# Kernel tuning notes

Measured on AMD Instinct MI355X. Metric: run time of the kernel, lower is better.

Reference implementation:

```python
import jax, jax.numpy as jnp
import numpy as np

EPS = 1e-5  # torch BatchNorm default eps


def _bn(x, gamma, beta, axes):
    # training-mode batch norm over `axes`, channel dim is axis 1
    mean = jnp.mean(x, axis=axes, keepdims=True)
    var = jnp.var(x, axis=axes, keepdims=True)
    shape = [1] * x.ndim
    shape[1] = -1
    return (x - mean) * jax.lax.rsqrt(var + EPS) * gamma.reshape(shape) + beta.reshape(shape)


def setup_inputs() -> dict:
    B, C, N = 16, 512, 192
    S_RATIO, R_RATIO = 4, 8
    Cs, Cr = C // S_RATIO, C // R_RATIO  # 128, 64
    inter = N * Cr + C  # 12800
    key = jax.random.key(0)
    ks = jax.random.split(key, 6)

    def w(k, shp, fan):
        return jax.random.normal(k, shp, jnp.float32) * np.float32(np.sqrt(2.0 / fan))

    return {
        "inputs": jax.random.normal(ks[0], (B, C, N), jnp.float32),
        "retain": 0,
        "theta_w": w(ks[1], (Cs, C), Cs), "theta_b": jnp.zeros((Cs,), jnp.float32),
        "theta_g": jnp.ones((Cs,), jnp.float32), "theta_be": jnp.zeros((Cs,), jnp.float32),
        "phi_w": w(ks[2], (Cs, C), Cs), "phi_b": jnp.zeros((Cs,), jnp.float32),
        "phi_g": jnp.ones((Cs,), jnp.float32), "phi_be": jnp.zeros((Cs,), jnp.float32),
        "re_w": w(ks[3], (Cr, Cs), Cr), "re_b": jnp.zeros((Cr,), jnp.float32),
        "re_g": jnp.ones((Cr,), jnp.float32), "re_be": jnp.zeros((Cr,), jnp.float32),
        "att_w": w(ks[4], (C, inter), C), "att_b": jnp.zeros((C,), jnp.float32),
        "att_g": jnp.ones((C,), jnp.float32), "att_be": jnp.zeros((C,), jnp.float32),
    }


def reference(inputs, retain, theta_w, theta_b, theta_g, theta_be,
              phi_w, phi_b, phi_g, phi_be, re_w, re_b, re_g, re_be,
              att_w, att_b, att_g, att_be):
    B, C, N = inputs.shape
    xt = inputs.transpose(0, 2, 1)  # [B, N, C]

    # theta / phi pro_blocks: Linear -> BN1d (over B,N) -> ReLU, output [B, Cs, N]
    th = jax.nn.relu(_bn(jnp.einsum('bnc,oc->bon', xt, theta_w) + theta_b[None, :, None], theta_g, theta_be, (0, 2)))
    ph = jax.nn.relu(_bn(jnp.einsum('bnc,oc->bon', xt, phi_w) + phi_b[None, :, None], phi_g, phi_be, (0, 2)))
    th = th.transpose(0, 2, 1)  # [B, N, Cs]
    ph = ph.transpose(0, 2, 1)  # [B, N, Cs]

    # pairwise broadcast-diff: [B, N, N, Cs]
    diff = th[:, :, None, :] - ph[:, None, :, :]

    # pro_block1: Linear -> BN2d -> ReLU, then flatten to [B, N, N*Cr]
    rel = jnp.einsum('bijc,oc->boij', diff, re_w) + re_b[None, :, None, None]  # [B, Cr, N, N]
    rel = jax.nn.relu(_bn(rel, re_g, re_be, (0, 2, 3)))
    rel = rel.transpose(0, 2, 3, 1).reshape(B, N, -1)  # [B, N, N*Cr]

    # attention_generator: Linear -> BN1d -> sigmoid, output [B, C, N]
    cat = jnp.concatenate([xt, rel], axis=2)  # [B, N, C + N*Cr]
    att = jnp.einsum('bni,oi->bon', cat, att_w) + att_b[None, :, None]  # [B, C, N]
    att = jax.nn.sigmoid(_bn(att, att_g, att_be, (0, 2)))

    features = att * inputs  # [B, C, N]
    if retain:
        return features
    return jnp.sum(features, axis=2) / jnp.sum(att, axis=2)  # [B, C]
```

## Files before the change

kernel.cpp:

```cpp
#include <hip/hip_runtime.h>

#define BB 16
#define CC 512
#define NN 192
#define CS 128
#define CR 64
#define EPSF 1e-5f
#define PART (BB*CC*NN)

typedef __attribute__((ext_vector_type(8))) short short8;
typedef __attribute__((ext_vector_type(4))) float f32x4;
typedef __attribute__((ext_vector_type(4))) unsigned int uint4v;

#define OFF_LIN2  0
#define OFF_P2    786432
#define OFF_QT    983040
#define OFF_ATTP4 1179648
#define OFF_WBF   7471104
#define OFF_XT    10747904
#define OFF_ROWS  11534336
#define OFF_SPART 11567104

__device__ __forceinline__ unsigned pkbf(float a, float b){
  unsigned r; asm("v_cvt_pk_bf16_f32 %0, %1, %2" : "=v"(r) : "v"(a), "v"(b)); return r;
}

__device__ __forceinline__ void gload_lds16(const void* g, void* l){
  __builtin_amdgcn_global_load_lds(
      (const __attribute__((address_space(1))) unsigned int*)g,
      (__attribute__((address_space(3))) unsigned int*)l, 16, 0, 0);
}

__global__ __launch_bounds__(256) void kconvxt(
    const float* __restrict__ aw, const float* __restrict__ x,
    short* __restrict__ wbf, short* __restrict__ xT)
{
  __shared__ float Ts[64][65];
  int tid = threadIdx.x;
  if (blockIdx.x < 3200) {
    int base = blockIdx.x * 2048;
    int i0 = base + tid*4;
    int i1 = base + 1024 + tid*4;
    float4 v0 = *reinterpret_cast<const float4*>(&aw[i0]);
    float4 v1 = *reinterpret_cast<const float4*>(&aw[i1]);
    uint2 w0 = make_uint2(pkbf(v0.x,v0.y), pkbf(v0.z,v0.w));
    uint2 w1 = make_uint2(pkbf(v1.x,v1.y), pkbf(v1.z,v1.w));
    *reinterpret_cast<uint2*>(&wbf[i0]) = w0;
    *reinterpret_cast<uint2*>(&wbf[i1]) = w1;
  } else {
    int bid = blockIdx.x - 3200;
    int nt = bid % 3; int ct = (bid/3) & 7; int b = bid / 24;
    int c0 = ct*64, n0 = nt*64;
    int col = tid & 63, r0 = tid >> 6;
    #pragma unroll
    for (int it = 0; it < 16; ++it){
      int r = r0 + it*4;
      Ts[r][col] = x[(b*CC + c0 + r)*NN + n0 + col];
    }
    __syncthreads();
    #pragma unroll
    for (int it = 0; it < 2; ++it){
      int cp = it*256 + tid;
      int nr = cp >> 3, cc8 = (cp & 7)*8;
      uint4v wv;
      wv.x = pkbf(Ts[cc8+0][nr], Ts[cc8+1][nr]);
      wv.y = pkbf(Ts[cc8+2][nr], Ts[cc8+3][nr]);
      wv.z = pkbf(Ts[cc8+4][nr], Ts[cc8+5][nr]);
      wv.w = pkbf(Ts[cc8+6][nr], Ts[cc8+7][nr]);
      *reinterpret_cast<uint4v*>(&xT[((b*NN) + n0 + nr)*CC + c0 + cc8]) = wv;
    }
  }
}

__global__ __launch_bounds__(256) void k1_lin(
    const float* __restrict__ x, const float* __restrict__ wth,
    const float* __restrict__ wph, float* __restrict__ lin2,
    float* __restrict__ spart)
{
  int bid = blockIdx.x;
  int nt = bid % 3; int ch = (bid/3) & 3; int b = (bid/12) & 15; int path = bid/192;
  int cs0 = ch*32, n0 = nt*64;
  const float* w = path ? wph : wth;
  int tid = threadIdx.x;
  int ty = tid >> 4, tx = tid & 15;
  __shared__ float Xs[32][64];
  __shared__ float Ws[32][36];
  float acc[2][4];
  #pragma unroll
  for (int i=0;i<2;++i)
    #pragma unroll
    for (int j=0;j<4;++j) acc[i][j]=0.f;
  for (int c0 = 0; c0 < CC; c0 += 32){
    __syncthreads();
    {
      int nn4 = (tid & 15)*4, cb = tid >> 4;
      *reinterpret_cast<float4*>(&Xs[cb][nn4]) =
        *reinterpret_cast<const float4*>(&x[(b*CC + c0 + cb)*NN + n0 + nn4]);
      *reinterpret_cast<float4*>(&Xs[cb+16][nn4]) =
        *reinterpret_cast<const float4*>(&x[(b*CC + c0 + cb + 16)*NN + n0 + nn4]);
    }
    {
      int cc = tid & 31, sb = tid >> 5;
      #pragma unroll
      for (int it = 0; it < 4; ++it)
        Ws[cc][sb + it*8] = w[(cs0 + sb + it*8)*CC + c0 + cc];
    }
    __syncthreads();
    #pragma unroll 8
    for (int cc = 0; cc < 32; ++cc){
      float w2[2], x4[4];
      w2[0] = Ws[cc][ty*2]; w2[1] = Ws[cc][ty*2+1];
      *reinterpret_cast<float4*>(x4) = *reinterpret_cast<const float4*>(&Xs[cc][tx*4]);
      #pragma unroll
      for (int i=0;i<2;++i)
        #pragma unroll
        for (int j=0;j<4;++j) acc[i][j] += w2[i]*x4[j];
    }
  }
  #pragma unroll
  for (int r = 0; r < 2; ++r){
    int cs = cs0 + ty*2 + r;
    float4 v = make_float4(acc[r][0],acc[r][1],acc[r][2],acc[r][3]);
    *reinterpret_cast<float4*>(&lin2[(b*256 + path*128 + cs)*NN + n0 + tx*4]) = v;
  }
  #pragma unroll
  for (int r = 0; r < 2; ++r){
    float s = acc[r][0]+acc[r][1]+acc[r][2]+acc[r][3];
    float q = acc[r][0]*acc[r][0]+acc[r][1]*acc[r][1]
            + acc[r][2]*acc[r][2]+acc[r][3]*acc[r][3];
    #pragma unroll
    for (int off=8; off; off>>=1){ s += __shfl_down(s,off,16); q += __shfl_down(q,off,16); }
    if (tx==0){
      int cs2 = path*128 + cs0 + ty*2 + r;
      spart[cs2*48 + b*3 + nt] = s;
      spart[12288 + cs2*48 + b*3 + nt] = q;
    }
  }
}

__global__ __launch_bounds__(256) void k3_gemm(
    const float* __restrict__ lin2, const float* __restrict__ spart,
    const float* __restrict__ tg, const float* __restrict__ tbe,
    const float* __restrict__ pg, const float* __restrict__ pbe,
    const float* __restrict__ rw,
    float* __restrict__ p2raw, float* __restrict__ qTraw,
    float* __restrict__ rows8)
{
  int bid = blockIdx.x;
  int ih = bid & 7; int b = (bid>>3) & 15; int path = bid >> 7;
  int i0 = ih*24;
  __shared__ float Ls[128][24];
  __shared__ float Ws[64][132];
  __shared__ float sscl[512];
  int tid = threadIdx.x;
  {
    int c2 = tid;
    float s=0.f, q=0.f;
    #pragma unroll 8
    for (int i=0;i<48;++i){ s += spart[c2*48+i]; q += spart[12288+c2*48+i]; }
    float mean = s * (1.f/3072.f);
    float var = q * (1.f/3072.f) - mean*mean;
    int pth = c2 >> 7, c = c2 & 127;
    float g  = pth ? pg[c]  : tg[c];
    float be = pth ? pbe[c] : tbe[c];
    float a = g * rsqrtf(var + EPSF);
    sscl[c2] = a; sscl[256+c2] = be - mean*a;
  }
  __syncthreads();
  #pragma unroll
  for (int it = 0; it < 3; ++it){
    int cp = it*256 + tid;
    int row = cp / 6, c4 = cp - row*6;
    float a = sscl[path*128 + row], d = sscl[256 + path*128 + row];
    float4 v = *reinterpret_cast<const float4*>(&lin2[(b*256 + path*128 + row)*NN + i0 + c4*4]);
    float4 r;
    r.x = fmaxf(a*v.x + d, 0.f); r.y = fmaxf(a*v.y + d, 0.f);
    r.z = fmaxf(a*v.z + d, 0.f); r.w = fmaxf(a*v.w + d, 0.f);
    *reinterpret_cast<float4*>(&Ls[row][c4*4]) = r;
  }
  #pragma unroll
  for (int it = 0; it < 8; ++it){
    int cp = it*256 + tid;
    int o = cp >> 5, c4 = cp & 31;
    *reinterpret_cast<float4*>(&Ws[o][c4*4]) =
      *reinterpret_cast<const float4*>(&rw[o*CS + c4*4]);
  }
  __syncthreads();
  int oy = tid >> 3, ix = tid & 7;
  float acc[2][3];
  #pragma unroll
  for (int r=0;r<2;++r)
    #pragma unroll
    for (int e=0;e<3;++e) acc[r][e]=0.f;
  #pragma unroll 4
  for (int c = 0; c < 128; ++c){
    float w2[2], l3[3];
    #pragma unroll
    for (int r=0;r<2;++r) w2[r] = Ws[oy*2+r][c];
    #pragma unroll
    for (int e=0;e<3;++e) l3[e] = Ls[c][ix*3+e];
    #pragma unroll
    for (int r=0;r<2;++r)
      #pragma unroll
      for (int e=0;e<3;++e) acc[r][e] += w2[r]*l3[e];
  }
  float* dst = path ? qTraw : p2raw;
  #pragma unroll
  for (int r=0;r<2;++r)
    #pragma unroll
    for (int e=0;e<3;++e)
      dst[(b*NN + i0 + ix*3 + e)*64 + oy*2 + r] = acc[r][e];
  #pragma unroll
  for (int r=0;r<2;++r){
    float s = acc[r][0]+acc[r][1]+acc[r][2];
    float q = acc[r][0]*acc[r][0]+acc[r][1]*acc[r][1]+acc[r][2]*acc[r][2];
    #pragma unroll
    for (int off=4; off; off>>=1){ s += __shfl_down(s,off,8); q += __shfl_down(q,off,8); }
    if (ix==0){
      int o = oy*2+r;
      int ri = (path*1024 + b*64 + o)*8 + ih;
      rows8[ri] = s; rows8[16384 + ri] = q;
    }
  }
}

__global__ __launch_bounds__(256) void k5_mfma(
    const short* __restrict__ wbf, const short* __restrict__ xT,
    const float* __restrict__ p2raw, const float* __restrict__ qTraw,
    const float* __restrict__ rows8,
    const float* __restrict__ rg, const float* __restrict__ rbe,
    unsigned short* __restrict__ attp4)
{
  int swz = (blockIdx.x & 7)*64 + (blockIdx.x >> 3);
  int nt = swz & 1, mt = (swz >> 1) & 3, b = (swz >> 3) & 15, ks = swz >> 7;
  int o20 = mt*128, n0 = nt*96;
  int j0 = ks*48;

  int tid = threadIdx.x;
  int w = tid >> 6, lane = tid & 63;
  int wr = w >> 1, wc = w & 1;
  int l15 = lane & 15, l4 = lane >> 4;
  int cq = tid & 7;

  __shared__ __align__(16) short As[2][128*64];
  __shared__ __align__(16) short Bs[96*64];
  __shared__ __align__(16) float qall[48*64];
  __shared__ float srel[128];
  __shared__ float sred[4][5][64];

  {
    int o = tid & 63, g = tid >> 6;
    float sa=0,sb=0,saq=0,sbq=0,cross=0;
    #pragma unroll
    for (int bb=g*4; bb<g*4+4; ++bb){
      float ra=0, rb=0;
      #pragma unroll
      for (int ih=0; ih<8; ++ih){
        int ia = (bb*64+o)*8 + ih, ib = (1024 + bb*64+o)*8 + ih;
        ra += rows8[ia]; rb += rows8[ib];
        saq += rows8[16384 + ia]; sbq += rows8[16384 + ib];
      }
      sa += ra; sb += rb; cross += ra*rb;
    }
    sred[g][0][o]=sa; sred[g][1][o]=sb; sred[g][2][o]=saq;
    sred[g][3][o]=sbq; sred[g][4][o]=cross;
  }
  {
    const float* qsrc = &qTraw[(size_t)(b*NN + j0)*64];
    #pragma unroll
    for (int it=0; it<3; ++it){
      int cp = it*256 + tid;
      gload_lds16(qsrc + cp*4, &qall[cp*4]);
    }
  }
  __syncthreads();
  if (tid < 64){
    int o = tid;
    float sa=0,sb=0,saq=0,sbq=0,cross=0;
    #pragma unroll
    for (int g=0; g<4; ++g){
      sa += sred[g][0][o]; sb += sred[g][1][o]; saq += sred[g][2][o];
      sbq += sred[g][3][o]; cross += sred[g][4][o];
    }
    float mean = (sa - sb) * (1.f/3072.f);
    float e2 = (saq + sbq) * (1.f/3072.f) - cross * (2.f/589824.f);
    float var = e2 - mean*mean;
    float s = rg[o] * rsqrtf(var + EPSF);
    srel[o] = s;
    srel[64+o] = rbe[o] - s*mean;
  }
  __syncthreads();

  float pr[3][8];
  {
    float sc8[8], sh8[8];
    #pragma unroll
    for (int k=0;k<8;++k){ sc8[k] = srel[cq*8+k]; sh8[k] = srel[64+cq*8+k]; }
    #pragma unroll
    for (int it=0; it<3; ++it){
      int n = it*32 + (tid >> 3);
      const float* pp = &p2raw[(size_t)((b*NN) + n0 + n)*64 + cq*8];
      float4 u0 = *reinterpret_cast<const float4*>(pp);
      float4 u1 = *reinterpret_cast<const float4*>(pp+4);
      pr[it][0]=sc8[0]*u0.x+sh8[0]; pr[it][1]=sc8[1]*u0.y+sh8[1];
      pr[it][2]=sc8[2]*u0.z+sh8[2]; pr[it][3]=sc8[3]*u0.w+sh8[3];
      pr[it][4]=sc8[4]*u1.x+sh8[4]; pr[it][5]=sc8[5]*u1.y+sh8[5];
      pr[it][6]=sc8[6]*u1.z+sh8[6]; pr[it][7]=sc8[7]*u1.w+sh8[7];
    }
  }

  auto stageA = [&](int buf, int colbase){
    #pragma unroll
    for (int it=0; it<4; ++it){
      int cp = w*256 + it*64 + lane;
      int row = cp >> 3, c = (cp & 7) ^ (row & 7);
      gload_lds16(&wbf[(o20 + row)*12800 + colbase + c*8],
                  &As[buf][(w*256 + it*64)*8]);
    }
  };
  auto stageBx = [&](int colbase){
    #pragma unroll
    for (int it=0; it<3; ++it){
      int cp = w*192 + it*64 + lane;
      int row = cp >> 3, c = (cp & 7) ^ (row & 7);
      gload_lds16(&xT[(size_t)((b*NN) + n0 + row)*CC + colbase + c*8],
                  &Bs[(w*192 + it*64)*8]);
    }
  };

  f32x4 acc[4][3];
  #pragma unroll
  for (int mi=0;mi<4;++mi)
    #pragma unroll
    for (int ni=0;ni<3;++ni) acc[mi][ni] = (f32x4){0.f,0.f,0.f,0.f};

  auto mfma_phase = [&](int buf){
    __builtin_amdgcn_s_setprio(1);
    #pragma unroll
    for (int s=0; s<2; ++s){
      short8 av[4], bv[3];
      int c = s*4 + l4;
      #pragma unroll
      for (int mi=0; mi<4; ++mi){
        int row = wr*64 + mi*16 + l15;
        av[mi] = *reinterpret_cast<const short8*>(&As[buf][row*64 + ((c ^ (row&7))<<3)]);
      }
      #pragma unroll
      for (int ni=0; ni<3; ++ni){
        int rown = wc*48 + ni*16 + l15;
        bv[ni] = *reinterpret_cast<const short8*>(&Bs[rown*64 + ((c ^ (rown&7))<<3)]);
      }
      #pragma unroll
      for (int mi=0; mi<4; ++mi)
        #pragma unroll
        for (int ni=0; ni<3; ++ni)
          acc[mi][ni] = __builtin_amdgcn_mfma_f32_16x16x32_bf16(av[mi], bv[ni], acc[mi][ni], 0, 0, 0);
    }
    __builtin_amdgcn_s_setprio(0);
  };

  #pragma unroll
  for (int kt = 0; kt < 2; ++kt){
    __syncthreads();
    stageA(0, ks*128 + kt*64);
    stageBx(ks*128 + kt*64);
    if (kt == 0){
      #pragma unroll
      for (int it=0; it<12; ++it){
        int i = it*256 + tid;
        qall[i] *= srel[i & 63];
      }
    }
    __syncthreads();
    mfma_phase(0);
  }

  __syncthreads();
  stageA(0, 512 + j0*64);
  for (int kt = 0; kt < 48; ++kt){
    int cur = kt & 1;
    if (kt < 47) stageA(cur^1, 512 + (j0 + kt + 1)*64);
    {
      const float* qq = &qall[kt*64];
      float4 qa = *reinterpret_cast<const float4*>(&qq[cq*8]);
      float4 qb = *reinterpret_cast<const float4*>(&qq[cq*8+4]);
      #pragma unroll
      for (int it=0; it<3; ++it){
        float r0 = fmaxf(pr[it][0]-qa.x, 0.f);
        float r1 = fmaxf(pr[it][1]-qa.y, 0.f);
        float r2 = fmaxf(pr[it][2]-qa.z, 0.f);
        float r3 = fmaxf(pr[it][3]-qa.w, 0.f);
        float r4 = fmaxf(pr[it][4]-qb.x, 0.f);
        float r5 = fmaxf(pr[it][5]-qb.y, 0.f);
        float r6 = fmaxf(pr[it][6]-qb.z, 0.f);
        float r7 = fmaxf(pr[it][7]-qb.w, 0.f);
        uint4v wv;
        wv.x = pkbf(r0,r1); wv.y = pkbf(r2,r3);
        wv.z = pkbf(r4,r5); wv.w = pkbf(r6,r7);
        int n = it*32 + (tid >> 3);
        *reinterpret_cast<uint4v*>(&Bs[n*64 + ((cq ^ (n&7))<<3)]) = wv;
      }
    }
    if (kt < 47) asm volatile("s_waitcnt vmcnt(4) lgkmcnt(0)" ::: "memory");
    else         asm volatile("s_waitcnt vmcnt(0) lgkmcnt(0)" ::: "memory");
    __builtin_amdgcn_sched_barrier(0);
    __builtin_amdgcn_s_barrier();
    mfma_phase(cur);
    __builtin_amdgcn_s_barrier();
  }

  unsigned short* dst = attp4 + (size_t)ks*PART;
  #pragma unroll
  for (int mi=0; mi<4; ++mi){
    #pragma unroll
    for (int r=0; r<4; ++r){
      int o2 = o20 + wr*64 + mi*16 + l4*4 + r;
      #pragma unroll
      for (int ni=0; ni<3; ++ni){
        int n = n0 + wc*48 + ni*16 + l15;
        dst[(b*CC + o2)*NN + n] = (unsigned short)pkbf(acc[mi][ni][r], 0.f);
      }
    }
  }
}

__global__ __launch_bounds__(256) void k67(
    const unsigned short* __restrict__ p4, const float* __restrict__ x,
    const float* __restrict__ g, const float* __restrict__ be,
    float* __restrict__ out)
{
  int o2 = blockIdx.x;
  int tid = threadIdx.x;
  int b = tid >> 4, nl = tid & 15;
  float v[12], xv[12];
  float s=0.f, q=0.f;
  #pragma unroll
  for (int it=0; it<6; ++it){
    int n = nl*2 + it*32;
    int idx = (b*CC + o2)*NN + n;
    float t0=0.f, t1=0.f;
    #pragma unroll
    for (int p=0; p<4; ++p){
      unsigned u = *reinterpret_cast<const unsigned*>(&p4[(size_t)p*PART + idx]);
      t0 += __uint_as_float(u << 16);
      t1 += __uint_as_float(u & 0xffff0000u);
    }
    float2 xu = *reinterpret_cast<const float2*>(&x[idx]);
    v[it*2] = t0; v[it*2+1] = t1;
    xv[it*2] = xu.x; xv[it*2+1] = xu.y;
    s += t0 + t1; q += t0*t0 + t1*t1;
  }
  __shared__ float rs[4], rq[4], ad[2];
  #pragma unroll
  for (int off=32; off; off>>=1){ s += __shfl_down(s,off); q += __shfl_down(q,off); }
  int w = tid >> 6;
  if ((tid & 63)==0){ rs[w]=s; rq[w]=q; }
  __syncthreads();
  if (tid==0){
    s = rs[0]+rs[1]+rs[2]+rs[3]; q = rq[0]+rq[1]+rq[2]+rq[3];
    float mean = s * (1.f/3072.f);
    float var = q * (1.f/3072.f) - mean*mean;
    float a = g[o2] * rsqrtf(var + EPSF);
    ad[0] = a; ad[1] = be[o2] - mean*a;
  }
  __syncthreads();
  float a = ad[0], d = ad[1];
  float sf=0.f, ss=0.f;
  #pragma unroll
  for (int it=0; it<12; ++it){
    float sig = 1.f/(1.f + expf(-(a*v[it] + d)));
    sf += sig * xv[it]; ss += sig;
  }
  #pragma unroll
  for (int off=8; off; off>>=1){ sf += __shfl_down(sf,off,16); ss += __shfl_down(ss,off,16); }
  if (nl==0) out[b*CC + o2] = sf/ss;
}

extern "C" void kernel_launch(void* const* d_in, const int* in_sizes, int n_in,
                              void* d_out, int out_size, void* d_ws, size_t ws_size,
                              hipStream_t stream)
{
  const float* inputs  = (const float*)d_in[0];
  const float* theta_w = (const float*)d_in[2];
  const float* theta_g = (const float*)d_in[4];
  const float* theta_be= (const float*)d_in[5];
  const float* phi_w   = (const float*)d_in[6];
  const float* phi_g   = (const float*)d_in[8];
  const float* phi_be  = (const float*)d_in[9];
  const float* re_w    = (const float*)d_in[10];
  const float* re_g    = (const float*)d_in[12];
  const float* re_be   = (const float*)d_in[13];
  const float* att_w   = (const float*)d_in[14];
  const float* att_g   = (const float*)d_in[16];
  const float* att_be  = (const float*)d_in[17];

  float* ws = (float*)d_ws;
  float* lin2  = ws + OFF_LIN2;
  float* p2raw = ws + OFF_P2;
  float* qTraw = ws + OFF_QT;
  unsigned short* attp4 = (unsigned short*)(ws + OFF_ATTP4);
  short* wbf   = (short*)(ws + OFF_WBF);
  short* xT    = (short*)(ws + OFF_XT);
  float* rows8 = ws + OFF_ROWS;
  float* spart = ws + OFF_SPART;

  kconvxt<<<3584, 256, 0, stream>>>(att_w, inputs, wbf, xT);
  k1_lin<<<384, 256, 0, stream>>>(inputs, theta_w, phi_w, lin2, spart);
  k3_gemm<<<256, 256, 0, stream>>>(lin2, spart, theta_g, theta_be, phi_g, phi_be,
                                   re_w, p2raw, qTraw, rows8);
  k5_mfma<<<512, 256, 0, stream>>>(wbf, xT, p2raw, qTraw, rows8, re_g, re_be, attp4);
  k67<<<512, 256, 0, stream>>>(attp4, inputs, att_g, att_be, (float*)d_out);
}
```

Before: 115.9 us.

## Increase split-K to six partitions and shrink LDS in relation GEMM

Splits the K dimension of the attention GEMM six ways instead of four, launching more blocks, each with a shorter relation loop, and unevenly distributing the input-channel tiles. It reuses the B tile buffer for reduction scratch to lower shared memory, and reorders the row-statistics layout for coalesced reads. It also prefetches the q tile earlier. The cost is extra bf16 partial-sum traffic and a wider reduction in the final kernel.

```diff
diff --git a/kernel.cpp b/kernel.cpp
--- a/kernel.cpp
+++ b/kernel.cpp
@@ -15,7 +15,7 @@
 #define OFF_LIN2  0
 #define OFF_P2    786432
 #define OFF_QT    983040
-#define OFF_ATTP4 1179648
+#define OFF_ATTP6 1179648
 #define OFF_WBF   7471104
 #define OFF_XT    10747904
 #define OFF_ROWS  11534336
@@ -218,7 +218,7 @@
     for (int off=4; off; off>>=1){ s += __shfl_down(s,off,8); q += __shfl_down(q,off,8); }
     if (ix==0){
       int o = oy*2+r;
-      int ri = (path*1024 + b*64 + o)*8 + ih;
+      int ri = ((path*8 + ih)*16 + b)*64 + o;
       rows8[ri] = s; rows8[16384 + ri] = q;
     }
   }
@@ -229,12 +229,14 @@
     const float* __restrict__ p2raw, const float* __restrict__ qTraw,
     const float* __restrict__ rows8,
     const float* __restrict__ rg, const float* __restrict__ rbe,
-    unsigned short* __restrict__ attp4)
+    unsigned short* __restrict__ attp6)
 {
-  int swz = (blockIdx.x & 7)*64 + (blockIdx.x >> 3);
+  int swz = (blockIdx.x & 7)*96 + (blockIdx.x >> 3);
   int nt = swz & 1, mt = (swz >> 1) & 3, b = (swz >> 3) & 15, ks = swz >> 7;
   int o20 = mt*128, n0 = nt*96;
-  int j0 = ks*48;
+  int j0 = ks*32;
+  int t0 = (ks < 2) ? ks*2 : ks + 2;
+  int xcnt = (ks < 2) ? 2 : 1;
 
   int tid = threadIdx.x;
   int w = tid >> 6, lane = tid & 63;
@@ -244,10 +246,15 @@
 
   __shared__ __align__(16) short As[2][128*64];
   __shared__ __align__(16) short Bs[96*64];
-  __shared__ __align__(16) float qall[48*64];
-  __shared__ float srel[128];
-  __shared__ float sred[4][5][64];
-
+  __shared__ __align__(16) float qall[32*64];
+  float* sredf = reinterpret_cast<float*>(Bs);
+  float* srelf = sredf + 1280;
+
+  {
+    const float* qsrc = &qTraw[(size_t)(b*NN + j0)*64];
+    gload_lds16(qsrc + tid*4, &qall[tid*4]);
+    gload_lds16(qsrc + (256+tid)*4, &qall[(256+tid)*4]);
+  }
   {
     int o = tid & 63, g = tid >> 6;
     float sa=0,sb=0,saq=0,sbq=0,cross=0;
@@ -256,22 +263,15 @@
       float ra=0, rb=0;
       #pragma unroll
       for (int ih=0; ih<8; ++ih){
-        int ia = (bb*64+o)*8 + ih, ib = (1024 + bb*64+o)*8 + ih;
+        int ia = (ih*16 + bb)*64 + o;
+        int ib = ((8+ih)*16 + bb)*64 + o;
         ra += rows8[ia]; rb += rows8[ib];
         saq += rows8[16384 + ia]; sbq += rows8[16384 + ib];
       }
       sa += ra; sb += rb; cross += ra*rb;
     }
-    sred[g][0][o]=sa; sred[g][1][o]=sb; sred[g][2][o]=saq;
-    sred[g][3][o]=sbq; sred[g][4][o]=cross;
-  }
-  {
-    const float* qsrc = &qTraw[(size_t)(b*NN + j0)*64];
-    #pragma unroll
-    for (int it=0; it<3; ++it){
-      int cp = it*256 + tid;
-      gload_lds16(qsrc + cp*4, &qall[cp*4]);
-    }
+    sredf[(g*5+0)*64+o]=sa; sredf[(g*5+1)*64+o]=sb; sredf[(g*5+2)*64+o]=saq;
+    sredf[(g*5+3)*64+o]=sbq; sredf[(g*5+4)*64+o]=cross;
   }
   __syncthreads();
   if (tid < 64){
@@ -279,23 +279,27 @@
     float sa=0,sb=0,saq=0,sbq=0,cross=0;
     #pragma unroll
     for (int g=0; g<4; ++g){
-      sa += sred[g][0][o]; sb += sred[g][1][o]; saq += sred[g][2][o];
-      sbq += sred[g][3][o]; cross += sred[g][4][o];
+      sa += sredf[(g*5+0)*64+o]; sb += sredf[(g*5+1)*64+o]; saq += sredf[(g*5+2)*64+o];
+      sbq += sredf[(g*5+3)*64+o]; cross += sredf[(g*5+4)*64+o];
     }
     float mean = (sa - sb) * (1.f/3072.f);
     float e2 = (saq + sbq) * (1.f/3072.f) - cross * (2.f/589824.f);
     float var = e2 - mean*mean;
     float s = rg[o] * rsqrtf(var + EPSF);
-    srel[o] = s;
-    srel[64+o] = rbe[o] - s*mean;
-  }
-  __syncthreads();
-
+    srelf[o] = s;
+    srelf[64+o] = rbe[o] - s*mean;
+  }
+  __syncthreads();
+  #pragma unroll
+  for (int it=0; it<8; ++it){
+    int i = it*256 + tid;
+    qall[i] *= srelf[i & 63];
+  }
   float pr[3][8];
   {
     float sc8[8], sh8[8];
     #pragma unroll
-    for (int k=0;k<8;++k){ sc8[k] = srel[cq*8+k]; sh8[k] = srel[64+cq*8+k]; }
+    for (int k=0;k<8;++k){ sc8[k] = srelf[cq*8+k]; sh8[k] = srelf[64+cq*8+k]; }
     #pragma unroll
     for (int it=0; it<3; ++it){
       int n = it*32 + (tid >> 3);
@@ -308,6 +312,7 @@
       pr[it][6]=sc8[6]*u1.z+sh8[6]; pr[it][7]=sc8[7]*u1.w+sh8[7];
     }
   }
+  __syncthreads();
 
   auto stageA = [&](int buf, int colbase){
     #pragma unroll
@@ -359,27 +364,18 @@
     __builtin_amdgcn_s_setprio(0);
   };
 
-  #pragma unroll
-  for (int kt = 0; kt < 2; ++kt){
-    __syncthreads();
-    stageA(0, ks*128 + kt*64);
-    stageBx(ks*128 + kt*64);
-    if (kt == 0){
-      #pragma unroll
-      for (int it=0; it<12; ++it){
-        int i = it*256 + tid;
-        qall[i] *= srel[i & 63];
-      }
-    }
+  for (int kt = 0; kt < xcnt; ++kt){
+    stageA(0, (t0 + kt)*64);
+    stageBx((t0 + kt)*64);
     __syncthreads();
     mfma_phase(0);
-  }
-
-  __syncthreads();
+    __syncthreads();
+  }
+
   stageA(0, 512 + j0*64);
-  for (int kt = 0; kt < 48; ++kt){
+  for (int kt = 0; kt < 32; ++kt){
     int cur = kt & 1;
-    if (kt < 47) stageA(cur^1, 512 + (j0 + kt + 1)*64);
+    if (kt < 31) stageA(cur^1, 512 + (j0 + kt + 1)*64);
     {
       const float* qq = &qall[kt*64];
       float4 qa = *reinterpret_cast<const float4*>(&qq[cq*8]);
@@ -401,7 +397,7 @@
         *reinterpret_cast<uint4v*>(&Bs[n*64 + ((cq ^ (n&7))<<3)]) = wv;
       }
     }
-    if (kt < 47) asm volatile("s_waitcnt vmcnt(4) lgkmcnt(0)" ::: "memory");
+    if (kt < 31) asm volatile("s_waitcnt vmcnt(4) lgkmcnt(0)" ::: "memory");
     else         asm volatile("s_waitcnt vmcnt(0) lgkmcnt(0)" ::: "memory");
     __builtin_amdgcn_sched_barrier(0);
     __builtin_amdgcn_s_barrier();
@@ -409,7 +405,7 @@
     __builtin_amdgcn_s_barrier();
   }
 
-  unsigned short* dst = attp4 + (size_t)ks*PART;
+  unsigned short* dst = attp6 + (size_t)ks*PART;
   #pragma unroll
   for (int mi=0; mi<4; ++mi){
     #pragma unroll
@@ -425,7 +421,7 @@
 }
 
 __global__ __launch_bounds__(256) void k67(
-    const unsigned short* __restrict__ p4, const float* __restrict__ x,
+    const unsigned short* __restrict__ p6, const float* __restrict__ x,
     const float* __restrict__ g, const float* __restrict__ be,
     float* __restrict__ out)
 {
@@ -440,8 +436,8 @@
     int idx = (b*CC + o2)*NN + n;
     float t0=0.f, t1=0.f;
     #pragma unroll
-    for (int p=0; p<4; ++p){
-      unsigned u = *reinterpret_cast<const unsigned*>(&p4[(size_t)p*PART + idx]);
+    for (int p=0; p<6; ++p){
+      unsigned u = *reinterpret_cast<const unsigned*>(&p6[(size_t)p*PART + idx]);
       t0 += __uint_as_float(u << 16);
       t1 += __uint_as_float(u & 0xffff0000u);
     }
@@ -498,7 +494,7 @@
   float* lin2  = ws + OFF_LIN2;
   float* p2raw = ws + OFF_P2;
   float* qTraw = ws + OFF_QT;
-  unsigned short* attp4 = (unsigned short*)(ws + OFF_ATTP4);
+  unsigned short* attp6 = (unsigned short*)(ws + OFF_ATTP6);
   short* wbf   = (short*)(ws + OFF_WBF);
   short* xT    = (short*)(ws + OFF_XT);
   float* rows8 = ws + OFF_ROWS;
@@ -508,6 +504,6 @@
   k1_lin<<<384, 256, 0, stream>>>(inputs, theta_w, phi_w, lin2, spart);
   k3_gemm<<<256, 256, 0, stream>>>(lin2, spart, theta_g, theta_be, phi_g, phi_be,
                                    re_w, p2raw, qTraw, rows8);
-  k5_mfma<<<512, 256, 0, stream>>>(wbf, xT, p2raw, qTraw, rows8, re_g, re_be, attp4);
-  k67<<<512, 256, 0, stream>>>(attp4, inputs, att_g, att_be, (float*)d_out);
-}
+  k5_mfma<<<768, 256, 0, stream>>>(wbf, xT, p2raw, qTraw, rows8, re_g, re_be, attp6);
+  k67<<<512, 256, 0, stream>>>(attp6, inputs, att_g, att_be, (float*)d_out);
+}
```

New measurement: 132.3 us. 1.14x slower.
